# Kernel tuning notes

Hardware: AMD Instinct MI355X
Metric: run time of the kernel (lower is better)

## Reference

```python
import jax, jax.numpy as jnp
import numpy as np

N_EMBD = 256
N_HEAD = 8
BATCH = 4
SEQ = 2048
NEG_BIAS = -1000000000.0


def setup_inputs() -> dict:
    key = jax.random.key(0)
    ks = jax.random.split(key, 5)
    scale = 1.0 / np.sqrt(N_EMBD)
    x = jax.random.normal(ks[0], (BATCH, SEQ, N_EMBD), dtype=jnp.float32)
    # torch Linear weight layout: (out_features, in_features)
    Wq = jax.random.normal(ks[1], (N_EMBD * N_HEAD, N_EMBD), dtype=jnp.float32) * scale
    Wk = jax.random.normal(ks[2], (N_EMBD * N_HEAD, N_EMBD), dtype=jnp.float32) * scale
    Wv = jax.random.normal(ks[3], (N_EMBD * N_HEAD, N_EMBD), dtype=jnp.float32) * scale
    Wo = jax.random.normal(ks[4], (N_EMBD, N_EMBD * N_HEAD), dtype=jnp.float32) * scale / np.sqrt(N_HEAD)
    return {"x": x, "Wq": Wq, "Wk": Wk, "Wv": Wv, "Wo": Wo}


def reference(x, Wq, Wk, Wv, Wo):
    B, L, E = x.shape
    H, D = N_HEAD, N_EMBD  # d_head == n_embd in this module
    # projections: x @ W.T, then split heads -> (B, H, L, D)
    def proj(W):
        y = jnp.einsum('ble,fe->blf', x, W)  # (B, L, H*D)
        return y.reshape(B, L, H, D).transpose(0, 2, 1, 3)
    q, k, v = proj(Wq), proj(Wk), proj(Wv)
    scores = jnp.einsum('bhld,bhmd->bhlm', q, k) * (E ** -0.5)
    # first (non-causal) softmax over full rows
    attn = jax.nn.softmax(scores, axis=-1)
    # causal mask replaces disallowed probs with large negative bias, then softmax again
    causal = jnp.tril(jnp.ones((L, L), dtype=bool))
    attn = jnp.where(causal[None, None], attn, jnp.asarray(NEG_BIAS, attn.dtype))
    attn = jax.nn.softmax(attn, axis=-1)
    out = jnp.einsum('bhlm,bhmd->bhld', attn, v)  # (B, H, L, D)
    out = out.transpose(0, 2, 1, 3).reshape(B, L, H * D)
    return jnp.einsum('blf,ef->ble', out, Wo)  # (B, L, E)
```

## Files before the change

### kernel.cpp

```cpp
#include <hip/hip_runtime.h>
#include <stdint.h>

typedef unsigned short ushort_t;
typedef __attribute__((ext_vector_type(8))) short bf16x8;
typedef __attribute__((ext_vector_type(4))) float f32x4;
typedef __attribute__((ext_vector_type(4))) unsigned short us4;

#define DEV __device__ __forceinline__

DEV ushort_t f2bf(float f) {
    unsigned int u = __float_as_uint(f);
    u += 0x7fffu + ((u >> 16) & 1u);
    return (ushort_t)(u >> 16);
}

DEV void async16(const ushort_t* g, ushort_t* l) {
    __builtin_amdgcn_global_load_lds(
        (const __attribute__((address_space(1))) void*)g,
        (__attribute__((address_space(3))) void*)l,
        16, 0, 0);
}

__global__ void convert_kernel(const float* __restrict__ x, const float* __restrict__ wq,
                               const float* __restrict__ wk, const float* __restrict__ wv,
                               const float* __restrict__ wo,
                               ushort_t* __restrict__ xb, ushort_t* __restrict__ wqb,
                               ushort_t* __restrict__ wkb, ushort_t* __restrict__ wvb,
                               ushort_t* __restrict__ wob)
{
    const int i = blockIdx.x * 256 + threadIdx.x;
    const float* src; ushort_t* dst; int off;
    if (i < 524288)      { src = x;  dst = xb;  off = i; }
    else if (i < 655360) { src = wq; dst = wqb; off = i - 524288; }
    else if (i < 786432) { src = wk; dst = wkb; off = i - 655360; }
    else if (i < 917504) { src = wv; dst = wvb; off = i - 786432; }
    else                 { src = wo; dst = wob; off = i - 917504; }
    const float4 v = ((const float4*)src)[off];
    us4 o;
    o[0] = f2bf(v.x); o[1] = f2bf(v.y); o[2] = f2bf(v.z); o[3] = f2bf(v.w);
    ((us4*)dst)[off] = o;
}

__global__ __launch_bounds__(256, 2) void qkv_gemm_kernel(
    const ushort_t* __restrict__ A, const ushort_t* __restrict__ wq,
    const ushort_t* __restrict__ wk, const ushort_t* __restrict__ wv,
    ushort_t* __restrict__ q_out, ushort_t* __restrict__ k_out,
    ushort_t* __restrict__ vt_out)
{
    __shared__ ushort_t At[128 * 64];
    __shared__ ushort_t Bt[128 * 64];

    const int K = 256, N = 2048;
    const int z = blockIdx.z;
    const ushort_t* Bm = (z == 0) ? wq : (z == 1) ? wk : wv;

    const int tid  = threadIdx.x;
    const int wave = tid >> 6;
    const int lane = tid & 63;
    const int quad = lane >> 4;
    const int l15  = lane & 15;
    const int mhalf = wave >> 1;
    const int nhalf = wave & 1;
    const int m0 = blockIdx.x * 128;
    const int n0 = blockIdx.y * 128;

    f32x4 acc[4][4];
#pragma unroll
    for (int mf = 0; mf < 4; ++mf)
#pragma unroll
        for (int nf = 0; nf < 4; ++nf)
#pragma unroll
            for (int r = 0; r < 4; ++r) acc[mf][nf][r] = 0.f;

    const int crow = (lane & 7) ^ (lane >> 3);

    for (int k0 = 0; k0 < K; k0 += 64) {
        __syncthreads();
#pragma unroll
        for (int t = 0; t < 4; ++t) {
            const int row = wave * 32 + t * 8 + (lane >> 3);
            async16(A + (size_t)(m0 + row) * K + k0 + crow * 8,
                    At + (wave * 32 + t * 8) * 64 + lane * 8);
            async16(Bm + (size_t)(n0 + row) * K + k0 + crow * 8,
                    Bt + (wave * 32 + t * 8) * 64 + lane * 8);
        }
        __syncthreads();
#pragma unroll
        for (int ks = 0; ks < 2; ++ks) {
            bf16x8 af[4], bf[4];
#pragma unroll
            for (int mf = 0; mf < 4; ++mf) {
                const int ml = mhalf * 64 + mf * 16 + l15;
                const int c = (ks * 4 + quad) ^ (ml & 7);
                af[mf] = *(const bf16x8*)(At + ml * 64 + c * 8);
            }
#pragma unroll
            for (int nf = 0; nf < 4; ++nf) {
                const int nl = nhalf * 64 + nf * 16 + l15;
                const int c = (ks * 4 + quad) ^ (nl & 7);
                bf[nf] = *(const bf16x8*)(Bt + nl * 64 + c * 8);
            }
#pragma unroll
            for (int mf = 0; mf < 4; ++mf)
#pragma unroll
                for (int nf = 0; nf < 4; ++nf)
                    acc[mf][nf] = __builtin_amdgcn_mfma_f32_16x16x32_bf16(
                        af[mf], bf[nf], acc[mf][nf], 0, 0, 0);
        }
    }

    if (z == 2) {
#pragma unroll
        for (int mf = 0; mf < 4; ++mf)
#pragma unroll
            for (int nf = 0; nf < 4; ++nf) {
                const int row = m0 + mhalf * 64 + mf * 16 + quad * 4;
                const int col = n0 + nhalf * 64 + nf * 16 + l15;
                const int b_ = row >> 11, l_ = row & 2047;
                const int h_ = col >> 8, d_ = col & 255;
                us4 pk;
#pragma unroll
                for (int r = 0; r < 4; ++r) pk[r] = f2bf(acc[mf][nf][r]);
                *(us4*)(vt_out + (((size_t)(b_ * 8 + h_) * 256 + d_) * 2048 + l_)) = pk;
            }
    } else {
        ushort_t* Cout = z ? k_out : q_out;
        const float sc = z ? 1.0f : 0.0625f;
#pragma unroll
        for (int mf = 0; mf < 4; ++mf)
#pragma unroll
            for (int nf = 0; nf < 4; ++nf)
#pragma unroll
                for (int r = 0; r < 4; ++r) {
                    const int row = m0 + mhalf * 64 + mf * 16 + quad * 4 + r;
                    const int col = n0 + nhalf * 64 + nf * 16 + l15;
                    Cout[(size_t)row * N + col] = f2bf(acc[mf][nf][r] * sc);
                }
    }
}

__global__ __launch_bounds__(256, 2) void out_gemm_splitk_kernel(
    const ushort_t* __restrict__ A, const ushort_t* __restrict__ Bm,
    float* __restrict__ Pout, int M, int N, int K)
{
    __shared__ ushort_t At[128 * 64];
    __shared__ ushort_t Bt[128 * 64];

    const int tid  = threadIdx.x;
    const int wave = tid >> 6;
    const int lane = tid & 63;
    const int quad = lane >> 4;
    const int l15  = lane & 15;
    const int mhalf = wave >> 1;
    const int nhalf = wave & 1;
    const int m0 = blockIdx.x * 128;
    const int n0 = blockIdx.y * 128;
    const int ks0 = blockIdx.z * 512;

    f32x4 acc[4][4];
#pragma unroll
    for (int mf = 0; mf < 4; ++mf)
#pragma unroll
        for (int nf = 0; nf < 4; ++nf)
#pragma unroll
            for (int r = 0; r < 4; ++r) acc[mf][nf][r] = 0.f;

    const int crow = (lane & 7) ^ (lane >> 3);

    for (int k0 = ks0; k0 < ks0 + 512; k0 += 64) {
        __syncthreads();
#pragma unroll
        for (int t = 0; t < 4; ++t) {
            const int row = wave * 32 + t * 8 + (lane >> 3);
            async16(A + (size_t)(m0 + row) * K + k0 + crow * 8,
                    At + (wave * 32 + t * 8) * 64 + lane * 8);
            async16(Bm + (size_t)(n0 + row) * K + k0 + crow * 8,
                    Bt + (wave * 32 + t * 8) * 64 + lane * 8);
        }
        __syncthreads();
#pragma unroll
        for (int ks = 0; ks < 2; ++ks) {
            bf16x8 af[4], bf[4];
#pragma unroll
            for (int mf = 0; mf < 4; ++mf) {
                const int ml = mhalf * 64 + mf * 16 + l15;
                const int c = (ks * 4 + quad) ^ (ml & 7);
                af[mf] = *(const bf16x8*)(At + ml * 64 + c * 8);
            }
#pragma unroll
            for (int nf = 0; nf < 4; ++nf) {
                const int nl = nhalf * 64 + nf * 16 + l15;
                const int c = (ks * 4 + quad) ^ (nl & 7);
                bf[nf] = *(const bf16x8*)(Bt + nl * 64 + c * 8);
            }
#pragma unroll
            for (int mf = 0; mf < 4; ++mf)
#pragma unroll
                for (int nf = 0; nf < 4; ++nf)
                    acc[mf][nf] = __builtin_amdgcn_mfma_f32_16x16x32_bf16(
                        af[mf], bf[nf], acc[mf][nf], 0, 0, 0);
        }
    }

    float* Cp = Pout + (size_t)blockIdx.z * M * N;
#pragma unroll
    for (int mf = 0; mf < 4; ++mf)
#pragma unroll
        for (int nf = 0; nf < 4; ++nf)
#pragma unroll
            for (int r = 0; r < 4; ++r) {
                const int row = m0 + mhalf * 64 + mf * 16 + quad * 4 + r;
                const int col = n0 + nhalf * 64 + nf * 16 + l15;
                Cp[(size_t)row * N + col] = acc[mf][nf][r];
            }
}

__global__ void reduce4_kernel(const float4* __restrict__ p, float4* __restrict__ out)
{
    const int i = blockIdx.x * 256 + threadIdx.x;
    float4 a = p[i];
    const float4 b = p[i + 524288];
    const float4 c = p[i + 1048576];
    const float4 d = p[i + 1572864];
    a.x += b.x + c.x + d.x;
    a.y += b.y + c.y + d.y;
    a.z += b.z + c.z + d.z;
    a.w += b.w + c.w + d.w;
    out[i] = a;
}

__global__ __launch_bounds__(256, 2) void out_gemm_kernel(
    const ushort_t* __restrict__ A, const ushort_t* __restrict__ Bm,
    float* __restrict__ Cout, int M, int N, int K)
{
    __shared__ ushort_t At[128 * 64];
    __shared__ ushort_t Bt[128 * 64];

    const int tid  = threadIdx.x;
    const int wave = tid >> 6;
    const int lane = tid & 63;
    const int quad = lane >> 4;
    const int l15  = lane & 15;
    const int mhalf = wave >> 1;
    const int nhalf = wave & 1;
    const int m0 = blockIdx.x * 128;
    const int n0 = blockIdx.y * 128;

    f32x4 acc[4][4];
#pragma unroll
    for (int mf = 0; mf < 4; ++mf)
#pragma unroll
        for (int nf = 0; nf < 4; ++nf)
#pragma unroll
            for (int r = 0; r < 4; ++r) acc[mf][nf][r] = 0.f;

    const int crow = (lane & 7) ^ (lane >> 3);

    for (int k0 = 0; k0 < K; k0 += 64) {
        __syncthreads();
#pragma unroll
        for (int t = 0; t < 4; ++t) {
            const int row = wave * 32 + t * 8 + (lane >> 3);
            async16(A + (size_t)(m0 + row) * K + k0 + crow * 8,
                    At + (wave * 32 + t * 8) * 64 + lane * 8);
            async16(Bm + (size_t)(n0 + row) * K + k0 + crow * 8,
                    Bt + (wave * 32 + t * 8) * 64 + lane * 8);
        }
        __syncthreads();
#pragma unroll
        for (int ks = 0; ks < 2; ++ks) {
            bf16x8 af[4], bf[4];
#pragma unroll
            for (int mf = 0; mf < 4; ++mf) {
                const int ml = mhalf * 64 + mf * 16 + l15;
                const int c = (ks * 4 + quad) ^ (ml & 7);
                af[mf] = *(const bf16x8*)(At + ml * 64 + c * 8);
            }
#pragma unroll
            for (int nf = 0; nf < 4; ++nf) {
                const int nl = nhalf * 64 + nf * 16 + l15;
                const int c = (ks * 4 + quad) ^ (nl & 7);
                bf[nf] = *(const bf16x8*)(Bt + nl * 64 + c * 8);
            }
#pragma unroll
            for (int mf = 0; mf < 4; ++mf)
#pragma unroll
                for (int nf = 0; nf < 4; ++nf)
                    acc[mf][nf] = __builtin_amdgcn_mfma_f32_16x16x32_bf16(
                        af[mf], bf[nf], acc[mf][nf], 0, 0, 0);
        }
    }

#pragma unroll
    for (int mf = 0; mf < 4; ++mf)
#pragma unroll
        for (int nf = 0; nf < 4; ++nf)
#pragma unroll
            for (int r = 0; r < 4; ++r) {
                const int row = m0 + mhalf * 64 + mf * 16 + quad * 4 + r;
                const int col = n0 + nhalf * 64 + nf * 16 + l15;
                Cout[(size_t)row * N + col] = acc[mf][nf][r];
            }
}

__global__ __launch_bounds__(256, 4) void pass1_kernel(
    const ushort_t* __restrict__ q_ws, const ushort_t* __restrict__ k_ws,
    float* __restrict__ rz_ws)
{
    __shared__ ushort_t Kt[64 * 256];
    __shared__ float zred[2][64];

    const int tid  = threadIdx.x;
    const int wave = tid >> 6;
    const int lane = tid & 63;
    const int quad = lane >> 4;
    const int l15  = lane & 15;
    const int ihalf = wave >> 1;
    const int jhalf = wave & 1;

    const int g  = blockIdx.x;
    const int bh = ((g >> 8) << 3) | (g & 7);
    const int it = (g >> 3) & 31;
    const int b = bh >> 3, h = bh & 7;
    const int i0 = it * 64;

    const size_t qkbase = (size_t)b * 2048 * 2048 + (size_t)h * 256;

    bf16x8 qf[2][8];
#pragma unroll
    for (int ng = 0; ng < 2; ++ng) {
        const int i_l = ihalf * 32 + ng * 16 + l15;
        const ushort_t* qr = q_ws + qkbase + (size_t)(i0 + i_l) * 2048;
#pragma unroll
        for (int ks = 0; ks < 8; ++ks)
            qf[ng][ks] = *(const bf16x8*)(qr + ks * 32 + quad * 8);
    }

    float z[2] = {0.f, 0.f};

    for (int jt = 0; jt < 32; ++jt) {
        const int j0 = jt * 64;
        __syncthreads();
        {
            const ushort_t* kb = k_ws + qkbase + (size_t)j0 * 2048;
#pragma unroll
            for (int t = 0; t < 8; ++t) {
                const int row = wave * 16 + t * 2 + (lane >> 5);
                const int c = (lane & 31) ^ (row & 7);
                async16(kb + (size_t)row * 2048 + c * 8,
                        Kt + (wave * 16 + t * 2) * 256 + lane * 8);
            }
        }
        __syncthreads();

        f32x4 sacc[2][2];
#pragma unroll
        for (int a = 0; a < 2; ++a)
#pragma unroll
            for (int c = 0; c < 2; ++c)
#pragma unroll
                for (int r = 0; r < 4; ++r) sacc[a][c][r] = 0.f;

        __builtin_amdgcn_s_setprio(1);
#pragma unroll
        for (int ks = 0; ks < 8; ++ks) {
            bf16x8 af[2];
#pragma unroll
            for (int mg = 0; mg < 2; ++mg) {
                const int j_l = jhalf * 32 + mg * 16 + l15;
                const int c = (ks * 4 + quad) ^ (j_l & 7);
                af[mg] = *(const bf16x8*)(Kt + j_l * 256 + c * 8);
            }
#pragma unroll
            for (int mg = 0; mg < 2; ++mg)
#pragma unroll
                for (int ng = 0; ng < 2; ++ng)
                    sacc[mg][ng] = __builtin_amdgcn_mfma_f32_16x16x32_bf16(
                        af[mg], qf[ng][ks], sacc[mg][ng], 0, 0, 0);
        }
        __builtin_amdgcn_s_setprio(0);

#pragma unroll
        for (int ng = 0; ng < 2; ++ng)
#pragma unroll
            for (int mg = 0; mg < 2; ++mg)
#pragma unroll
                for (int r = 0; r < 4; ++r)
                    z[ng] += __expf(sacc[mg][ng][r]);
    }

#pragma unroll
    for (int ng = 0; ng < 2; ++ng) {
        z[ng] += __shfl_xor(z[ng], 16);
        z[ng] += __shfl_xor(z[ng], 32);
    }
    __syncthreads();
    if (quad == 0) {
#pragma unroll
        for (int ng = 0; ng < 2; ++ng) {
            const int i_l = ihalf * 32 + ng * 16 + l15;
            zred[jhalf][i_l] = z[ng];
        }
    }
    __syncthreads();
    if (tid < 64)
        rz_ws[(size_t)bh * 2048 + i0 + tid] = 1.0f / (zred[0][tid] + zred[1][tid]);
}

__global__ __launch_bounds__(256, 2) void pass2_kernel(
    const ushort_t* __restrict__ q_ws, const ushort_t* __restrict__ k_ws,
    const ushort_t* __restrict__ vt_ws, const float* __restrict__ rz_ws,
    ushort_t* __restrict__ attn_out)
{
    __shared__ ushort_t smem[36864];
    ushort_t* Kt = smem;
    ushort_t* Vt = smem + 16384;
    ushort_t* Wt = smem + 32768;

    const int tid  = threadIdx.x;
    const int wave = tid >> 6;
    const int lane = tid & 63;
    const int quad = lane >> 4;
    const int l15  = lane & 15;
    const int ihalf = wave >> 1;
    const int jhalf = wave & 1;

    const int g  = blockIdx.x;
    const int bh = ((g >> 8) << 3) | (g & 7);
    const int it = 31 - ((g >> 3) & 31);
    const int b = bh >> 3, h = bh & 7;
    const int i0 = it * 64;

    const size_t qkbase = (size_t)b * 2048 * 2048 + (size_t)h * 256;

    bf16x8 qf[2][8];
#pragma unroll
    for (int ng = 0; ng < 2; ++ng) {
        const int i_l = ihalf * 32 + ng * 16 + l15;
        const ushort_t* qr = q_ws + qkbase + (size_t)(i0 + i_l) * 2048;
#pragma unroll
        for (int ks = 0; ks < 8; ++ks)
            qf[ng][ks] = *(const bf16x8*)(qr + ks * 32 + quad * 8);
    }

    float rzrow[2];
#pragma unroll
    for (int ng = 0; ng < 2; ++ng) {
        const int i_l = ihalf * 32 + ng * 16 + l15;
        rzrow[ng] = rz_ws[(size_t)bh * 2048 + i0 + i_l];
    }

    f32x4 oacc[2][8];
#pragma unroll
    for (int mg = 0; mg < 2; ++mg)
#pragma unroll
        for (int nf = 0; nf < 8; ++nf)
#pragma unroll
            for (int r = 0; r < 4; ++r) oacc[mg][nf][r] = 0.f;
    float den[2] = {0.f, 0.f};

    for (int jt = 0; jt <= it; ++jt) {
        const int j0 = jt * 64;
        const bool diag = (jt == it);
        __syncthreads();
        {
            const ushort_t* kb = k_ws + qkbase + (size_t)j0 * 2048;
#pragma unroll
            for (int t = 0; t < 8; ++t) {
                const int row = wave * 16 + t * 2 + (lane >> 5);
                const int c = (lane & 31) ^ (row & 7);
                async16(kb + (size_t)row * 2048 + c * 8,
                        Kt + (wave * 16 + t * 2) * 256 + lane * 8);
            }
            const ushort_t* vb = vt_ws + (size_t)bh * 256 * 2048 + j0;
#pragma unroll
            for (int t = 0; t < 8; ++t) {
                const int row = wave * 64 + t * 8 + (lane >> 3);
                const int c = (lane & 7) ^ (row & 7);
                async16(vb + (size_t)row * 2048 + c * 8,
                        Vt + (wave * 64 + t * 8) * 64 + lane * 8);
            }
        }
        __syncthreads();

        f32x4 sacc[2][2];
#pragma unroll
        for (int a = 0; a < 2; ++a)
#pragma unroll
            for (int c = 0; c < 2; ++c)
#pragma unroll
                for (int r = 0; r < 4; ++r) sacc[a][c][r] = 0.f;

#pragma unroll
        for (int ks = 0; ks < 8; ++ks) {
            bf16x8 af[2];
#pragma unroll
            for (int mg = 0; mg < 2; ++mg) {
                const int j_l = jhalf * 32 + mg * 16 + l15;
                const int c = (ks * 4 + quad) ^ (j_l & 7);
                af[mg] = *(const bf16x8*)(Kt + j_l * 256 + c * 8);
            }
#pragma unroll
            for (int mg = 0; mg < 2; ++mg)
#pragma unroll
                for (int ng = 0; ng < 2; ++ng)
                    sacc[mg][ng] = __builtin_amdgcn_mfma_f32_16x16x32_bf16(
                        af[mg], qf[ng][ks], sacc[mg][ng], 0, 0, 0);
        }

#pragma unroll
        for (int mg = 0; mg < 2; ++mg) {
#pragma unroll
            for (int ng = 0; ng < 2; ++ng) {
                const int i_l = ihalf * 32 + ng * 16 + l15;
                const int jb = jhalf * 32 + mg * 16 + quad * 4;
                us4 wp;
#pragma unroll
                for (int r = 0; r < 4; ++r) {
                    const float p = __expf(sacc[mg][ng][r]) * rzrow[ng];
                    float w = __expf(p);
                    if (diag && (jb + r > i_l)) w = 0.f;
                    den[ng] += w;
                    wp[r] = f2bf(w);
                }
                const int c = (jb >> 3) ^ (i_l & 7);
                *(us4*)(Wt + i_l * 64 + c * 8 + (jb & 7)) = wp;
            }
        }
        __syncthreads();

#pragma unroll
        for (int ks = 0; ks < 2; ++ks) {
            bf16x8 aw[2];
#pragma unroll
            for (int mg = 0; mg < 2; ++mg) {
                const int i_l = ihalf * 32 + mg * 16 + l15;
                const int c = (ks * 4 + quad) ^ (i_l & 7);
                aw[mg] = *(const bf16x8*)(Wt + i_l * 64 + c * 8);
            }
#pragma unroll
            for (int nf = 0; nf < 8; ++nf) {
                const int d = jhalf * 128 + nf * 16 + l15;
                const int c = (ks * 4 + quad) ^ (d & 7);
                const bf16x8 bv = *(const bf16x8*)(Vt + d * 64 + c * 8);
                oacc[0][nf] = __builtin_amdgcn_mfma_f32_16x16x32_bf16(aw[0], bv, oacc[0][nf], 0, 0, 0);
                oacc[1][nf] = __builtin_amdgcn_mfma_f32_16x16x32_bf16(aw[1], bv, oacc[1][nf], 0, 0, 0);
            }
        }
    }

    __syncthreads();
    {
        float* dbuf = (float*)Kt;
#pragma unroll
        for (int ng = 0; ng < 2; ++ng) {
            const int i_l = ihalf * 32 + ng * 16 + l15;
            dbuf[(jhalf * 4 + quad) * 64 + i_l] = den[ng];
        }
    }
    __syncthreads();
    if (tid < 64) {
        const float* dbuf = (const float*)Kt;
        float s = 0.f;
#pragma unroll
        for (int p = 0; p < 8; ++p) s += dbuf[p * 64 + tid];
        ((float*)Kt)[512 + tid] = 1.0f / s;
    }
    __syncthreads();
    {
        const float* rden = (const float*)Kt + 512;
#pragma unroll
        for (int mg = 0; mg < 2; ++mg) {
#pragma unroll
            for (int r = 0; r < 4; ++r) {
                const int i_l = ihalf * 32 + mg * 16 + quad * 4 + r;
                const float rd = rden[i_l];
                ushort_t* orow = attn_out + qkbase + (size_t)(i0 + i_l) * 2048;
#pragma unroll
                for (int nf = 0; nf < 8; ++nf) {
                    const int d = jhalf * 128 + nf * 16 + l15;
                    orow[d] = f2bf(oacc[mg][nf][r] * rd);
                }
            }
        }
    }
}

extern "C" void kernel_launch(void* const* d_in, const int* in_sizes, int n_in,
                              void* d_out, int out_size, void* d_ws, size_t ws_size,
                              hipStream_t stream) {
    const float* x  = (const float*)d_in[0];
    const float* Wq = (const float*)d_in[1];
    const float* Wk = (const float*)d_in[2];
    const float* Wv = (const float*)d_in[3];
    const float* Wo = (const float*)d_in[4];

    char* ws = (char*)d_ws;
    ushort_t* xb    = (ushort_t*)(ws);
    ushort_t* wqb   = (ushort_t*)(ws + 4194304);
    ushort_t* wkb   = (ushort_t*)(ws + 5242880);
    ushort_t* wvb   = (ushort_t*)(ws + 6291456);
    ushort_t* wob   = (ushort_t*)(ws + 7340032);
    ushort_t* q_ws  = (ushort_t*)(ws + 8388608);
    ushort_t* k_ws  = (ushort_t*)(ws + 41943040);
    ushort_t* vt_ws = (ushort_t*)(ws + 75497472);
    ushort_t* ao_ws = (ushort_t*)(ws + 109051904);
    float*    rz_ws = (float*)   (ws + 142606336);

    const size_t PG_OFF = 142868480ull;
    const size_t PG_END = PG_OFF + 33554432ull;
    const bool use_splitk = ws_size >= PG_END;
    float* pg_ws = (float*)(ws + PG_OFF);

    convert_kernel<<<4096, 256, 0, stream>>>(x, Wq, Wk, Wv, Wo, xb, wqb, wkb, wvb, wob);

    qkv_gemm_kernel<<<dim3(64, 16, 3), 256, 0, stream>>>(
        xb, wqb, wkb, wvb, q_ws, k_ws, vt_ws);

    pass1_kernel<<<1024, 256, 0, stream>>>(q_ws, k_ws, rz_ws);
    pass2_kernel<<<1024, 256, 0, stream>>>(q_ws, k_ws, vt_ws, rz_ws, ao_ws);

    if (use_splitk) {
        out_gemm_splitk_kernel<<<dim3(64, 2, 4), 256, 0, stream>>>(
            ao_ws, wob, pg_ws, 8192, 256, 2048);
        reduce4_kernel<<<2048, 256, 0, stream>>>(
            (const float4*)pg_ws, (float4*)d_out);
    } else {
        out_gemm_kernel<<<dim3(64, 2), 256, 0, stream>>>(
            ao_ws, wob, (float*)d_out, 8192, 256, 2048);
    }
}
```

Baseline: 361.3 us.

## Double attention query tile to 128 rows with 512-thread blocks and paired scheduling

```diff
diff --git a/kernel.cpp b/kernel.cpp
--- a/kernel.cpp
+++ b/kernel.cpp
@@ -303,33 +303,34 @@
             }
 }
 
-__global__ __launch_bounds__(256, 4) void pass1_kernel(
+__global__ __launch_bounds__(512, 4) void pass1_kernel(
     const ushort_t* __restrict__ q_ws, const ushort_t* __restrict__ k_ws,
     float* __restrict__ rz_ws)
 {
     __shared__ ushort_t Kt[64 * 256];
-    __shared__ float zred[2][64];
+    __shared__ float zred[2][128];
 
     const int tid  = threadIdx.x;
     const int wave = tid >> 6;
     const int lane = tid & 63;
     const int quad = lane >> 4;
     const int l15  = lane & 15;
-    const int ihalf = wave >> 1;
+    const int iq    = wave >> 1;
     const int jhalf = wave & 1;
 
     const int g  = blockIdx.x;
-    const int bh = ((g >> 8) << 3) | (g & 7);
-    const int it = (g >> 3) & 31;
-    const int b = bh >> 3, h = bh & 7;
-    const int i0 = it * 64;
+    const int h  = g & 7;
+    const int b  = (g >> 3) & 3;
+    const int it = g >> 5;
+    const int bh = b * 8 + h;
+    const int i0 = it * 128;
 
     const size_t qkbase = (size_t)b * 2048 * 2048 + (size_t)h * 256;
 
     bf16x8 qf[2][8];
 #pragma unroll
     for (int ng = 0; ng < 2; ++ng) {
-        const int i_l = ihalf * 32 + ng * 16 + l15;
+        const int i_l = iq * 32 + ng * 16 + l15;
         const ushort_t* qr = q_ws + qkbase + (size_t)(i0 + i_l) * 2048;
 #pragma unroll
         for (int ks = 0; ks < 8; ++ks)
@@ -339,16 +340,15 @@
     float z[2] = {0.f, 0.f};
 
     for (int jt = 0; jt < 32; ++jt) {
-        const int j0 = jt * 64;
         __syncthreads();
         {
-            const ushort_t* kb = k_ws + qkbase + (size_t)j0 * 2048;
-#pragma unroll
-            for (int t = 0; t < 8; ++t) {
-                const int row = wave * 16 + t * 2 + (lane >> 5);
+            const ushort_t* kb = k_ws + qkbase + (size_t)jt * 64 * 2048;
+#pragma unroll
+            for (int t = 0; t < 4; ++t) {
+                const int row = wave * 8 + t * 2 + (lane >> 5);
                 const int c = (lane & 31) ^ (row & 7);
                 async16(kb + (size_t)row * 2048 + c * 8,
-                        Kt + (wave * 16 + t * 2) * 256 + lane * 8);
+                        Kt + (wave * 8 + t * 2) * 256 + lane * 8);
             }
         }
         __syncthreads();
@@ -398,21 +398,21 @@
     if (quad == 0) {
 #pragma unroll
         for (int ng = 0; ng < 2; ++ng) {
-            const int i_l = ihalf * 32 + ng * 16 + l15;
+            const int i_l = iq * 32 + ng * 16 + l15;
             zred[jhalf][i_l] = z[ng];
         }
     }
     __syncthreads();
-    if (tid < 64)
+    if (tid < 128)
         rz_ws[(size_t)bh * 2048 + i0 + tid] = 1.0f / (zred[0][tid] + zred[1][tid]);
 }
 
-__global__ __launch_bounds__(256, 2) void pass2_kernel(
+__global__ __launch_bounds__(512, 2) void pass2_kernel(
     const ushort_t* __restrict__ q_ws, const ushort_t* __restrict__ k_ws,
     const ushort_t* __restrict__ vt_ws, const float* __restrict__ rz_ws,
     ushort_t* __restrict__ attn_out)
 {
-    __shared__ ushort_t smem[36864];
+    __shared__ ushort_t smem[40960];
     ushort_t* Kt = smem;
     ushort_t* Vt = smem + 16384;
     ushort_t* Wt = smem + 32768;
@@ -422,21 +422,23 @@
     const int lane = tid & 63;
     const int quad = lane >> 4;
     const int l15  = lane & 15;
-    const int ihalf = wave >> 1;
+    const int iq    = wave >> 1;
     const int jhalf = wave & 1;
 
     const int g  = blockIdx.x;
-    const int bh = ((g >> 8) << 3) | (g & 7);
-    const int it = 31 - ((g >> 3) & 31);
-    const int b = bh >> 3, h = bh & 7;
-    const int i0 = it * 64;
+    const int h  = g & 7;
+    const int b  = (g >> 3) & 3;
+    const int x  = g >> 5;
+    const int it = (x < 8) ? (2 * x) : (31 - 2 * x);
+    const int bh = b * 8 + h;
+    const int i0 = it * 128;
 
     const size_t qkbase = (size_t)b * 2048 * 2048 + (size_t)h * 256;
 
     bf16x8 qf[2][8];
 #pragma unroll
     for (int ng = 0; ng < 2; ++ng) {
-        const int i_l = ihalf * 32 + ng * 16 + l15;
+        const int i_l = iq * 32 + ng * 16 + l15;
         const ushort_t* qr = q_ws + qkbase + (size_t)(i0 + i_l) * 2048;
 #pragma unroll
         for (int ks = 0; ks < 8; ++ks)
@@ -446,7 +448,7 @@
     float rzrow[2];
 #pragma unroll
     for (int ng = 0; ng < 2; ++ng) {
-        const int i_l = ihalf * 32 + ng * 16 + l15;
+        const int i_l = iq * 32 + ng * 16 + l15;
         rzrow[ng] = rz_ws[(size_t)bh * 2048 + i0 + i_l];
     }
 
@@ -459,26 +461,27 @@
             for (int r = 0; r < 4; ++r) oacc[mg][nf][r] = 0.f;
     float den[2] = {0.f, 0.f};
 
-    for (int jt = 0; jt <= it; ++jt) {
+    const int jmax = 2 * it + 1;
+    for (int jt = 0; jt <= jmax; ++jt) {
         const int j0 = jt * 64;
-        const bool diag = (jt == it);
+        const int jzone = jt - 2 * it;
         __syncthreads();
         {
             const ushort_t* kb = k_ws + qkbase + (size_t)j0 * 2048;
 #pragma unroll
-            for (int t = 0; t < 8; ++t) {
-                const int row = wave * 16 + t * 2 + (lane >> 5);
+            for (int t = 0; t < 4; ++t) {
+                const int row = wave * 8 + t * 2 + (lane >> 5);
                 const int c = (lane & 31) ^ (row & 7);
                 async16(kb + (size_t)row * 2048 + c * 8,
-                        Kt + (wave * 16 + t * 2) * 256 + lane * 8);
+                        Kt + (wave * 8 + t * 2) * 256 + lane * 8);
             }
             const ushort_t* vb = vt_ws + (size_t)bh * 256 * 2048 + j0;
 #pragma unroll
-            for (int t = 0; t < 8; ++t) {
-                const int row = wave * 64 + t * 8 + (lane >> 3);
+            for (int t = 0; t < 4; ++t) {
+                const int row = wave * 32 + t * 8 + (lane >> 3);
                 const int c = (lane & 7) ^ (row & 7);
                 async16(vb + (size_t)row * 2048 + c * 8,
-                        Vt + (wave * 64 + t * 8) * 64 + lane * 8);
+                        Vt + (wave * 32 + t * 8) * 64 + lane * 8);
             }
         }
         __syncthreads();
@@ -512,14 +515,14 @@
         for (int mg = 0; mg < 2; ++mg) {
 #pragma unroll
             for (int ng = 0; ng < 2; ++ng) {
-                const int i_l = ihalf * 32 + ng * 16 + l15;
+                const int i_l = iq * 32 + ng * 16 + l15;
                 const int jb = jhalf * 32 + mg * 16 + quad * 4;
                 us4 wp;
 #pragma unroll
                 for (int r = 0; r < 4; ++r) {
                     const float p = __expf(sacc[mg][ng][r]) * rzrow[ng];
                     float w = __expf(p);
-                    if (diag && (jb + r > i_l)) w = 0.f;
+                    if (jzone >= 0 && (jzone * 64 + jb + r > i_l)) w = 0.f;
                     den[ng] += w;
                     wp[r] = f2bf(w);
                 }
@@ -534,7 +537,7 @@
             bf16x8 aw[2];
 #pragma unroll
             for (int mg = 0; mg < 2; ++mg) {
-                const int i_l = ihalf * 32 + mg * 16 + l15;
+                const int i_l = iq * 32 + mg * 16 + l15;
                 const int c = (ks * 4 + quad) ^ (i_l & 7);
                 aw[mg] = *(const bf16x8*)(Wt + i_l * 64 + c * 8);
             }
@@ -554,26 +557,26 @@
         float* dbuf = (float*)Kt;
 #pragma unroll
         for (int ng = 0; ng < 2; ++ng) {
-            const int i_l = ihalf * 32 + ng * 16 + l15;
-            dbuf[(jhalf * 4 + quad) * 64 + i_l] = den[ng];
+            const int i_l = iq * 32 + ng * 16 + l15;
+            dbuf[(jhalf * 4 + quad) * 128 + i_l] = den[ng];
         }
     }
     __syncthreads();
-    if (tid < 64) {
+    if (tid < 128) {
         const float* dbuf = (const float*)Kt;
         float s = 0.f;
 #pragma unroll
-        for (int p = 0; p < 8; ++p) s += dbuf[p * 64 + tid];
-        ((float*)Kt)[512 + tid] = 1.0f / s;
+        for (int p = 0; p < 8; ++p) s += dbuf[p * 128 + tid];
+        ((float*)Kt)[1024 + tid] = 1.0f / s;
     }
     __syncthreads();
     {
-        const float* rden = (const float*)Kt + 512;
+        const float* rden = (const float*)Kt + 1024;
 #pragma unroll
         for (int mg = 0; mg < 2; ++mg) {
 #pragma unroll
             for (int r = 0; r < 4; ++r) {
-                const int i_l = ihalf * 32 + mg * 16 + quad * 4 + r;
+                const int i_l = iq * 32 + mg * 16 + quad * 4 + r;
                 const float rd = rden[i_l];
                 ushort_t* orow = attn_out + qkbase + (size_t)(i0 + i_l) * 2048;
 #pragma unroll
@@ -617,8 +620,8 @@
     qkv_gemm_kernel<<<dim3(64, 16, 3), 256, 0, stream>>>(
         xb, wqb, wkb, wvb, q_ws, k_ws, vt_ws);
 
-    pass1_kernel<<<1024, 256, 0, stream>>>(q_ws, k_ws, rz_ws);
-    pass2_kernel<<<1024, 256, 0, stream>>>(q_ws, k_ws, vt_ws, rz_ws, ao_ws);
+    pass1_kernel<<<512, 512, 0, stream>>>(q_ws, k_ws, rz_ws);
+    pass2_kernel<<<512, 512, 0, stream>>>(q_ws, k_ws, vt_ws, rz_ws, ao_ws);
 
     if (use_splitk) {
         out_gemm_splitk_kernel<<<dim3(64, 2, 4), 256, 0, stream>>>(
```

New measurement: 308.1 us, median of 2. 1.17x faster.
